# Kernel tuning notes

Measured on AMD Instinct MI355X. Metric: run time of the kernel, lower is better.

The kernel has to match this reference:

```python
import jax, jax.numpy as jnp
import numpy as np

B, S, D, H, F = 4, 1024, 1024, 16, 4096
DH = D // H
EPS = 1e-5


def _ln(x, g, b):
    mu = jnp.mean(x, axis=-1, keepdims=True)
    var = jnp.mean((x - mu) ** 2, axis=-1, keepdims=True)
    return (x - mu) * jax.lax.rsqrt(var + EPS) * g + b


def _mha(q_in, k_in, v_in, mask, wq, bq, wk, bk, wv, bv, wo, bo):
    b, sq, d = q_in.shape
    sk = k_in.shape[1]
    Q = (q_in @ wq + bq).reshape(b, sq, H, DH).transpose(0, 2, 1, 3)  # [B,H,Sq,dh]
    K = (k_in @ wk + bk).reshape(b, sk, H, DH).transpose(0, 2, 1, 3)
    V = (v_in @ wv + bv).reshape(b, sk, H, DH).transpose(0, 2, 1, 3)
    scores = jnp.einsum('bhqd,bhkd->bhqk', Q, K) / jnp.sqrt(jnp.asarray(DH, Q.dtype))
    if mask is not None:
        scores = jnp.where(mask[:, None] == 0, jnp.asarray(-1e9, scores.dtype), scores)
    w = jax.nn.softmax(scores, axis=-1)
    ctx = jnp.einsum('bhqk,bhkd->bhqd', w, V).transpose(0, 2, 1, 3).reshape(b, sq, d)
    return ctx @ wo + bo


def setup_inputs() -> dict:
    key = jax.random.key(0)
    ks = jax.random.split(key, 20)
    s = 0.02
    inp = {
        'x': jax.random.normal(ks[0], (B, S, D), jnp.float32),
        'src_x': jax.random.normal(ks[1], (B, S, D), jnp.float32),
        # causal self-attention mask (1 = keep), cross mask all ones
        'mask': jnp.broadcast_to(jnp.tril(jnp.ones((S, S), jnp.int32)), (B, S, S)),
        'src_mask': jnp.ones((B, S, S), jnp.int32),
        'ln1_g': jnp.ones((D,), jnp.float32), 'ln1_b': jnp.zeros((D,), jnp.float32),
        'ln2_g': jnp.ones((D,), jnp.float32), 'ln2_b': jnp.zeros((D,), jnp.float32),
        'ln3_g': jnp.ones((D,), jnp.float32), 'ln3_b': jnp.zeros((D,), jnp.float32),
    }
    names = ['sa_wq', 'sa_wk', 'sa_wv', 'sa_wo', 'ca_wq', 'ca_wk', 'ca_wv', 'ca_wo']
    for i, n in enumerate(names):
        inp[n] = jax.random.normal(ks[2 + i], (D, D), jnp.float32) * s
        inp[n.replace('w', 'b')] = jnp.zeros((D,), jnp.float32)
    inp['ff_w1'] = jax.random.normal(ks[10], (D, F), jnp.float32) * s
    inp['ff_b1'] = jnp.zeros((F,), jnp.float32)
    inp['ff_w2'] = jax.random.normal(ks[11], (F, D), jnp.float32) * s
    inp['ff_b2'] = jnp.zeros((D,), jnp.float32)
    return inp


def reference(x, mask, src_x, src_mask,
              ln1_g, ln1_b, ln2_g, ln2_b, ln3_g, ln3_b,
              sa_wq, sa_bq, sa_wk, sa_bk, sa_wv, sa_bv, sa_wo, sa_bo,
              ca_wq, ca_bq, ca_wk, ca_bk, ca_wv, ca_bv, ca_wo, ca_bo,
              ff_w1, ff_b1, ff_w2, ff_b2):
    # pre-layer-norm decoder layer (dropout = 0 / eval mode)
    h = _ln(x, ln1_g, ln1_b)
    x = x + _mha(h, h, h, mask, sa_wq, sa_bq, sa_wk, sa_bk, sa_wv, sa_bv, sa_wo, sa_bo)
    h = _ln(x, ln2_g, ln2_b)
    x = x + _mha(h, src_x, src_x, src_mask, ca_wq, ca_bq, ca_wk, ca_bk, ca_wv, ca_bv, ca_wo, ca_bo)
    h = _ln(x, ln3_g, ln3_b)
    x = x + (jax.nn.relu(h @ ff_w1 + ff_b1) @ ff_w2 + ff_b2)
    return x
```

## Files before the change

### kernel.cpp

```cpp
#include <hip/hip_runtime.h>
#include <hip/hip_bf16.h>

#define B_ 4
#define S_ 1024
#define D_ 1024
#define H_ 16
#define DH_ 64
#define F_ 4096

typedef unsigned short u16;
typedef unsigned int u32;
typedef __attribute__((ext_vector_type(8))) short bf16x8;
typedef __attribute__((ext_vector_type(4))) short bf16x4;
typedef __attribute__((ext_vector_type(4))) float f32x4;

__device__ __forceinline__ float bf2f(u16 u) {
    return __uint_as_float(((u32)u) << 16);
}
__device__ __forceinline__ u16 f2bf(float f) {
    __hip_bfloat16 h = __float2bfloat16(f);
    return *reinterpret_cast<u16*>(&h);
}

typedef __attribute__((address_space(1))) const u32 gu32;
typedef __attribute__((address_space(3))) u32 lu32;
__device__ __forceinline__ void gl_lds16(const void* g, void* l) {
    __builtin_amdgcn_global_load_lds((gu32*)g, (lu32*)l, 16, 0, 0);
}

__global__ __launch_bounds__(256) void cvt1_kernel(const float* __restrict__ s,
                                                   u16* __restrict__ d) {
    int i = (blockIdx.x * 256 + threadIdx.x) * 4;
    float4 v = *(const float4*)(s + i);
    u16 o0 = f2bf(v.x), o1 = f2bf(v.y), o2 = f2bf(v.z), o3 = f2bf(v.w);
    d[i] = o0; d[i+1] = o1; d[i+2] = o2; d[i+3] = o3;
}

__device__ __forceinline__ void trcvt_body(const float* __restrict__ src,
                                           u16* __restrict__ dst, int K, int N,
                                           int n0, int k0) {
    __shared__ u16 tile[64][65];
    int t = threadIdx.x;
    int c = t & 63, r4 = t >> 6;
#pragma unroll
    for (int i = 0; i < 16; i++) {
        int r = i * 4 + r4;
        tile[c][r] = f2bf(src[(size_t)(k0 + r) * N + n0 + c]);
    }
    __syncthreads();
#pragma unroll
    for (int i = 0; i < 16; i++) {
        int rr = i * 4 + r4;
        dst[(size_t)(n0 + rr) * K + k0 + c] = tile[rr][c];
    }
}

__global__ __launch_bounds__(256) void trcvt_kernel(const float* __restrict__ src,
                                                    u16* __restrict__ dst,
                                                    int K, int N) {
    trcvt_body(src, dst, K, N, blockIdx.x * 64, blockIdx.y * 64);
}

struct TP { const float* src[8]; u16* dst[8]; };
__global__ __launch_bounds__(256) void trcvt8_kernel(TP tp) {
    trcvt_body(tp.src[blockIdx.z], tp.dst[blockIdx.z], D_, D_,
               blockIdx.x * 64, blockIdx.y * 64);
}

__global__ __launch_bounds__(256) void mask_reduce_kernel(const int* __restrict__ mask,
                                                          unsigned char* __restrict__ bmask) {
    int t = threadIdx.x;
    int qb = blockIdx.x >> 4, kb = blockIdx.x & 15, b = blockIdx.y;
    bool all1 = true, any1 = false;
#pragma unroll
    for (int i = 0; i < 16; i++) {
        int e = t + i * 256;
        int r = e >> 6, c = e & 63;
        int v = mask[((size_t)(b * S_ + qb * 64 + r)) * S_ + kb * 64 + c];
        all1 = all1 && (v != 0);
        any1 = any1 || (v != 0);
    }
    unsigned long long ba = __ballot(all1), bn = __ballot(any1);
    __shared__ unsigned long long sa[4], sn[4];
    if ((t & 63) == 0) { sa[t >> 6] = ba; sn[t >> 6] = bn; }
    __syncthreads();
    if (t == 0) {
        bool A = ((sa[0] & sa[1] & sa[2] & sa[3]) == ~0ull);
        bool Y = ((sn[0] | sn[1] | sn[2] | sn[3]) != 0ull);
        bmask[b * 256 + blockIdx.x] = A ? 2 : (Y ? 1 : 0);
    }
}

template<bool COPY>
__global__ __launch_bounds__(256) void ln_kernel(const float* __restrict__ xin,
                                                 const float* __restrict__ g,
                                                 const float* __restrict__ bta,
                                                 float* xcur,
                                                 u16* __restrict__ hout) {
    int row = blockIdx.x;
    int t = threadIdx.x;
    size_t base = (size_t)row * D_;
    float v[4];
#pragma unroll
    for (int i = 0; i < 4; i++) v[i] = xin[base + t + i * 256];
    float s  = v[0] + v[1] + v[2] + v[3];
    float s2 = v[0]*v[0] + v[1]*v[1] + v[2]*v[2] + v[3]*v[3];
#pragma unroll
    for (int m = 1; m < 64; m <<= 1) {
        s  += __shfl_xor(s, m);
        s2 += __shfl_xor(s2, m);
    }
    __shared__ float red[8];
    int wave = t >> 6;
    if ((t & 63) == 0) { red[wave*2] = s; red[wave*2+1] = s2; }
    __syncthreads();
    float fs  = red[0] + red[2] + red[4] + red[6];
    float fs2 = red[1] + red[3] + red[5] + red[7];
    float mu  = fs * (1.0f / D_);
    float var = fs2 * (1.0f / D_) - mu * mu;
    float rs  = rsqrtf(var + 1e-5f);
#pragma unroll
    for (int i = 0; i < 4; i++) {
        int c = t + i * 256;
        float x = v[i];
        if (COPY) xcur[base + c] = x;
        hout[base + c] = f2bf((x - mu) * rs * g[c] + bta[c]);
    }
}

struct Bias3 { const float* b0; const float* b1; const float* b2; int n1; int n2; };

__device__ __forceinline__ float bias_at(const Bias3& bs, int c) {
    const float* p; int o;
    if (c < bs.n1)      { p = bs.b0; o = c; }
    else if (c < bs.n2) { p = bs.b1; o = c - bs.n1; }
    else                { p = bs.b2; o = c - bs.n2; }
    return p[o];
}

template<int BM, int BN, int OUT_MODE, bool BIAS_ROW>
__global__ __launch_bounds__(256) void gemm128_kernel(const u16* __restrict__ A,
                                                      const u16* __restrict__ Bt,
                                                      Bias3 bias,
                                                      const float* res,
                                                      void* out,
                                                      int M, int N, int K) {
    constexpr int MT = (BM == 64) ? 4 : (BN == 64 ? 2 : 4);
    constexpr int NT = (BN == 64) ? 4 : (BM == 64 ? 2 : 4);
    __shared__ u16 As[2][BM * 64];
    __shared__ u16 Bs[2][BN * 64];
    int t = threadIdx.x;
    int m0 = blockIdx.y * BM, n0 = blockIdx.x * BN;
    int w = t >> 6, lane = t & 63, quad = lane >> 4, l16 = lane & 15;
    int wm, wn;
    if (BM == 128 && BN == 128) { wm = (w >> 1) * 64; wn = (w & 1) * 64; }
    else if (BN == 64)          { wm = w * 32;        wn = 0; }
    else                        { wm = 0;             wn = w * 32; }

    f32x4 acc[MT][NT] = {};
    int sr = lane >> 3;
    int gc = ((lane & 7) ^ sr) * 8;
    int x7 = l16 & 7;
    const u16* gA = A + (size_t)m0 * K;
    const u16* gB = Bt + (size_t)n0 * K;

    auto stage = [&](int k0, int buf) {
#pragma unroll
        for (int j = w; j < BM / 8; j += 4)
            gl_lds16(gA + (size_t)(j * 8 + sr) * K + k0 + gc, &As[buf][j * 512]);
#pragma unroll
        for (int j = w; j < BN / 8; j += 4)
            gl_lds16(gB + (size_t)(j * 8 + sr) * K + k0 + gc, &Bs[buf][j * 512]);
    };

    stage(0, 0);
    int cur = 0;
    for (int k0 = 0; k0 < K; k0 += 64) {
        __syncthreads();
        if (k0 + 64 < K) stage(k0 + 64, cur ^ 1);

#pragma unroll
        for (int s = 0; s < 2; s++) {
            bf16x8 af[MT], bfr[NT];
            int cp = ((s * 4 + quad) ^ x7) * 8;
#pragma unroll
            for (int mt = 0; mt < MT; mt++)
                af[mt] = *(const bf16x8*)&As[cur][(wm + mt * 16 + l16) * 64 + cp];
#pragma unroll
            for (int nt = 0; nt < NT; nt++)
                bfr[nt] = *(const bf16x8*)&Bs[cur][(wn + nt * 16 + l16) * 64 + cp];
#pragma unroll
            for (int mt = 0; mt < MT; mt++)
#pragma unroll
                for (int nt = 0; nt < NT; nt++)
                    acc[mt][nt] = __builtin_amdgcn_mfma_f32_16x16x32_bf16(af[mt], bfr[nt], acc[mt][nt], 0, 0, 0);
        }
        cur ^= 1;
    }

#pragma unroll
    for (int nt = 0; nt < NT; nt++) {
        int col = n0 + wn + nt * 16 + l16;
        float bc = BIAS_ROW ? 0.f : bias_at(bias, col);
#pragma unroll
        for (int mt = 0; mt < MT; mt++) {
#pragma unroll
            for (int r = 0; r < 4; r++) {
                int row = m0 + wm + mt * 16 + quad * 4 + r;
                float v = acc[mt][nt][r] + (BIAS_ROW ? bias_at(bias, row) : bc);
                if (OUT_MODE == 1) v = fmaxf(v, 0.f);
                if (OUT_MODE == 2) {
                    v += res[(size_t)row * N + col];
                    ((float*)out)[(size_t)row * N + col] = v;
                } else {
                    ((u16*)out)[(size_t)row * N + col] = f2bf(v);
                }
            }
        }
    }
}

__global__ __launch_bounds__(256) void attn_kernel(const u16* __restrict__ Q, int ldq,
                                                   const u16* __restrict__ Kb, int ldk,
                                                   const u16* __restrict__ Vt,
                                                   const int* __restrict__ mask,
                                                   const unsigned char* __restrict__ bmask,
                                                   u16* __restrict__ ctx) {
    __shared__ u16 Ks[2][2][64 * 64];
    __shared__ u16 Vs[2][2][64 * 64];
    int t = threadIdx.x;
    int b = blockIdx.z, hh = blockIdx.y;
    int w = t >> 6, lane = t & 63, quad = lane >> 4, l16 = lane & 15;
    int hoff = hh * DH_;

    int qt[2] = { (int)blockIdx.x, 15 - (int)blockIdx.x };

    bf16x8 ones8;
#pragma unroll
    for (int j = 0; j < 8; j++) ones8[j] = (short)0x3F80;

    bf16x8 qf[2][2];
#pragma unroll
    for (int tt = 0; tt < 2; tt++) {
        int qrow = qt[tt] * 64 + w * 16 + l16;
#pragma unroll
        for (int kk = 0; kk < 2; kk++) {
            bf16x8 v = *(const bf16x8*)(Q + (size_t)(b * S_ + qrow) * ldq + hoff + kk * 32 + quad * 8);
#pragma unroll
            for (int j = 0; j < 8; j++)
                v[j] = (short)f2bf(bf2f((u16)v[j]) * 0.125f);
            qf[tt][kk] = v;
        }
    }

    f32x4 oacc[2][4] = {};
    f32x4 lacc[2] = {};

    unsigned nz[2], mx[2];
#pragma unroll
    for (int tt = 0; tt < 2; tt++) {
        nz[tt] = 0; mx[tt] = 0;
        for (int c = 0; c < 16; c++) {
            int v = bmask ? (int)bmask[(b * 16 + qt[tt]) * 16 + c] : 1;
            if (v)      nz[tt] |= 1u << c;
            if (v == 1) mx[tt] |= 1u << c;
        }
    }
    unsigned nzU = nz[0] | nz[1];
    unsigned remS = 0;
    for (int s = 0; s < 8; s++) if ((nzU >> (2 * s)) & 3u) remS |= 1u << s;

    int sr = lane >> 3;
    int gc = ((lane & 7) ^ sr) * 8;

    auto stage64 = [&](int c, int buf) {
        int k0 = c * 64, c64 = c & 1;
        for (int j = w; j < 8; j += 4) {
            gl_lds16(Kb + (size_t)(b * S_ + k0 + j * 8 + sr) * ldk + hoff + gc, &Ks[buf][c64][j * 512]);
            gl_lds16(Vt + (size_t)(hoff + j * 8 + sr) * (B_ * S_) + b * S_ + k0 + gc, &Vs[buf][c64][j * 512]);
        }
    };
    auto stageS = [&](int s, int buf) {
        if ((nzU >> (2 * s)) & 1u)     stage64(2 * s, buf);
        if ((nzU >> (2 * s + 1)) & 1u) stage64(2 * s + 1, buf);
    };

    int cur = 0;
    int s = remS ? __builtin_ctz(remS) : 8;
    if (s < 8) stageS(s, 0);

    while (s < 8) {
        remS &= remS - 1;
        int ns = remS ? __builtin_ctz(remS) : 8;
        __syncthreads();
        if (ns < 8) stageS(ns, cur ^ 1);

#pragma unroll
        for (int c64 = 0; c64 < 2; c64++) {
            int c = 2 * s + c64;
            if (!((nzU >> c) & 1u)) continue;
            int k0c = c * 64;
            const u16* KsT = &Ks[cur][c64][0];
            const u16* VsT = &Vs[cur][c64][0];

#pragma unroll
            for (int tt = 0; tt < 2; tt++) {
                if (!((nz[tt] >> c) & 1u)) continue;
                bool mixed = (mx[tt] >> c) & 1u;

                float p[4][4];
#pragma unroll
                for (int nt = 0; nt < 4; nt++) {
                    f32x4 sacc = {};
                    int krow = nt * 16 + l16;
#pragma unroll
                    for (int kk = 0; kk < 2; kk++) {
                        int cp = ((kk * 4 + quad) ^ (krow & 7)) * 8;
                        bf16x8 kf = *(const bf16x8*)&KsT[krow * 64 + cp];
                        sacc = __builtin_amdgcn_mfma_f32_16x16x32_bf16(kf, qf[tt][kk], sacc, 0, 0, 0);
                    }
#pragma unroll
                    for (int r = 0; r < 4; r++) {
                        float sv = sacc[r];
                        if (mixed) {
                            int qq = qt[tt] * 64 + w * 16 + l16;
                            int kc = k0c + nt * 16 + quad * 4 + r;
                            if (mask[(size_t)(b * S_ + qq) * S_ + kc] == 0) sv = -1e9f;
                        }
                        p[nt][r] = __expf(fminf(sv, 20.f));
                    }
                }

#pragma unroll
                for (int mp = 0; mp < 2; mp++) {
                    bf16x8 af;
#pragma unroll
                    for (int r = 0; r < 4; r++) {
                        af[r]     = (short)f2bf(p[2 * mp][r]);
                        af[4 + r] = (short)f2bf(p[2 * mp + 1][r]);
                    }
                    lacc[tt] = __builtin_amdgcn_mfma_f32_16x16x32_bf16(af, ones8, lacc[tt], 0, 0, 0);
#pragma unroll
                    for (int dt = 0; dt < 4; dt++) {
                        int vrow = dt * 16 + l16;
                        int ch0 = ((2 * mp) * 2 + (quad >> 1)) ^ (vrow & 7);
                        int ch1 = ((2 * mp + 1) * 2 + (quad >> 1)) ^ (vrow & 7);
                        int off = (quad & 1) * 4;
                        bf16x4 lo = *(const bf16x4*)&VsT[vrow * 64 + ch0 * 8 + off];
                        bf16x4 hi = *(const bf16x4*)&VsT[vrow * 64 + ch1 * 8 + off];
                        bf16x8 vf;
#pragma unroll
                        for (int j = 0; j < 4; j++) { vf[j] = lo[j]; vf[4 + j] = hi[j]; }
                        oacc[tt][dt] = __builtin_amdgcn_mfma_f32_16x16x32_bf16(af, vf, oacc[tt][dt], 0, 0, 0);
                    }
                }
            }
        }
        s = ns;
        cur ^= 1;
    }

#pragma unroll
    for (int tt = 0; tt < 2; tt++)
#pragma unroll
        for (int dt = 0; dt < 4; dt++)
#pragma unroll
            for (int r = 0; r < 4; r++) {
                int qq = qt[tt] * 64 + w * 16 + quad * 4 + r;
                float l = lacc[tt][r];
                float inv = l > 0.f ? 1.f / l : 0.f;
                ctx[(size_t)(b * S_ + qq) * D_ + hoff + dt * 16 + l16] = f2bf(oacc[tt][dt][r] * inv);
            }
}

extern "C" void kernel_launch(void* const* d_in, const int* in_sizes, int n_in,
                              void* d_out, int out_size, void* d_ws, size_t ws_size,
                              hipStream_t stream) {
    const float* x     = (const float*)d_in[0];
    const float* srcx  = (const float*)d_in[1];
    const int*   mask  = (const int*)d_in[2];
    const int*   smask = (const int*)d_in[3];
    const float* ln1g = (const float*)d_in[4],  *ln1b = (const float*)d_in[5];
    const float* ln2g = (const float*)d_in[6],  *ln2b = (const float*)d_in[7];
    const float* ln3g = (const float*)d_in[8],  *ln3b = (const float*)d_in[9];
    const float* sa_wq = (const float*)d_in[10], *sa_bq = (const float*)d_in[11];
    const float* sa_wk = (const float*)d_in[12], *sa_bk = (const float*)d_in[13];
    const float* sa_wv = (const float*)d_in[14], *sa_bv = (const float*)d_in[15];
    const float* sa_wo = (const float*)d_in[16], *sa_bo = (const float*)d_in[17];
    const float* ca_wq = (const float*)d_in[18], *ca_bq = (const float*)d_in[19];
    const float* ca_wk = (const float*)d_in[20], *ca_bk = (const float*)d_in[21];
    const float* ca_wv = (const float*)d_in[22], *ca_bv = (const float*)d_in[23];
    const float* ca_wo = (const float*)d_in[24], *ca_bo = (const float*)d_in[25];
    const float* ff_w1 = (const float*)d_in[26], *ff_b1 = (const float*)d_in[27];
    const float* ff_w2 = (const float*)d_in[28], *ff_b2 = (const float*)d_in[29];

    char* ws = (char*)d_ws;
    const size_t MB = 1ull << 20;
    const size_t DD = (size_t)D_ * D_;
    float* xcur = (float*)ws;
    u16* h     = (u16*)(ws + 16 * MB);
    u16* qk    = (u16*)(ws + 24 * MB);
    u16* qb    = (u16*)(ws + 24 * MB);
    u16* kbuf  = (u16*)(ws + 32 * MB);
    u16* vt    = (u16*)(ws + 40 * MB);
    u16* ctx   = (u16*)(ws + 48 * MB);
    u16* ff    = (u16*)(ws + 24 * MB);
    u16* sxb   = (u16*)(ws + 56 * MB);
    u16* wqk_s = (u16*)(ws + 64 * MB);
    u16* wv_s  = (u16*)(ws + 68 * MB);
    u16* wo_s  = (u16*)(ws + 70 * MB);
    u16* wq_c  = (u16*)(ws + 72 * MB);
    u16* wk_c  = (u16*)(ws + 74 * MB);
    u16* wv_c  = (u16*)(ws + 76 * MB);
    u16* wo_c  = (u16*)(ws + 78 * MB);
    u16* wff1  = (u16*)(ws + 80 * MB);
    u16* wff2  = (u16*)(ws + 88 * MB);
    unsigned char* bm_self = nullptr, *bm_cross = nullptr;
    if (ws_size >= 96 * MB + 8192) {
        bm_self  = (unsigned char*)(ws + ws_size - 8192);
        bm_cross = bm_self + 4096;
    }

    dim3 blk(256);

    TP tp = {{sa_wq, sa_wk, sa_wv, sa_wo, ca_wq, ca_wk, ca_wv, ca_wo},
             {wqk_s, wqk_s + DD, wv_s, wo_s, wq_c, wk_c, wv_c, wo_c}};
    trcvt8_kernel<<<dim3(16, 16, 8), blk, 0, stream>>>(tp);
    trcvt_kernel<<<dim3(F_ / 64, D_ / 64), blk, 0, stream>>>(ff_w1, wff1, D_, F_);
    trcvt_kernel<<<dim3(D_ / 64, F_ / 64), blk, 0, stream>>>(ff_w2, wff2, F_, D_);
    cvt1_kernel<<<B_ * S_ * D_ / 1024, blk, 0, stream>>>(srcx, sxb);
    if (bm_self) {
        mask_reduce_kernel<<<dim3(256, B_), blk, 0, stream>>>(mask, bm_self);
        mask_reduce_kernel<<<dim3(256, B_), blk, 0, stream>>>(smask, bm_cross);
    }

    Bias3 bqk = { sa_bq, sa_bk, sa_bk, 1024, 2048 };
    Bias3 bsv = { sa_bv, sa_bv, sa_bv, 1 << 30, 1 << 30 };
    Bias3 bso = { sa_bo, sa_bo, sa_bo, 1 << 30, 1 << 30 };
    Bias3 bcq = { ca_bq, ca_bq, ca_bq, 1 << 30, 1 << 30 };
    Bias3 bck = { ca_bk, ca_bk, ca_bk, 1 << 30, 1 << 30 };
    Bias3 bcv = { ca_bv, ca_bv, ca_bv, 1 << 30, 1 << 30 };
    Bias3 bco = { ca_bo, ca_bo, ca_bo, 1 << 30, 1 << 30 };
    Bias3 bf1 = { ff_b1, ff_b1, ff_b1, 1 << 30, 1 << 30 };
    Bias3 bf2 = { ff_b2, ff_b2, ff_b2, 1 << 30, 1 << 30 };

    ln_kernel<true><<<B_ * S_, blk, 0, stream>>>(x, ln1g, ln1b, xcur, h);
    gemm128_kernel<128,128,0,false><<<dim3(16, 32), blk, 0, stream>>>(h, wqk_s, bqk, nullptr, qk, 4096, 2048, 1024);
    gemm128_kernel<64,128,0,true><<<dim3(32, 16), blk, 0, stream>>>(wv_s, h, bsv, nullptr, vt, 1024, 4096, 1024);
    attn_kernel<<<dim3(8, H_, B_), blk, 0, stream>>>(qk, 2048, qk + 1024, 2048, vt, mask, bm_self, ctx);
    gemm128_kernel<128,64,2,false><<<dim3(16, 32), blk, 0, stream>>>(ctx, wo_s, bso, xcur, xcur, 4096, 1024, 1024);

    ln_kernel<false><<<B_ * S_, blk, 0, stream>>>(xcur, ln2g, ln2b, nullptr, h);
    gemm128_kernel<128,64,0,false><<<dim3(16, 32), blk, 0, stream>>>(h, wq_c, bcq, nullptr, qb, 4096, 1024, 1024);
    gemm128_kernel<128,64,0,false><<<dim3(16, 32), blk, 0, stream>>>(sxb, wk_c, bck, nullptr, kbuf, 4096, 1024, 1024);
    gemm128_kernel<64,128,0,true><<<dim3(32, 16), blk, 0, stream>>>(wv_c, sxb, bcv, nullptr, vt, 1024, 4096, 1024);
    attn_kernel<<<dim3(8, H_, B_), blk, 0, stream>>>(qb, 1024, kbuf, 1024, vt, smask, bm_cross, ctx);
    gemm128_kernel<128,64,2,false><<<dim3(16, 32), blk, 0, stream>>>(ctx, wo_c, bco, xcur, xcur, 4096, 1024, 1024);

    ln_kernel<false><<<B_ * S_, blk, 0, stream>>>(xcur, ln3g, ln3b, nullptr, h);
    gemm128_kernel<128,128,1,false><<<dim3(32, 32), blk, 0, stream>>>(h, wff1, bf1, nullptr, ff, 4096, 4096, 1024);
    gemm128_kernel<128,64,2,false><<<dim3(16, 32), blk, 0, stream>>>(ff, wff2, bf2, xcur, (float*)d_out, 4096, 1024, 4096);
}
```

Baseline: 575.8 us.

## Split-K the FFN2 GEMM, batch cross Q/K GEMMs, add MFMA priority hints

The FFN down-projection (K=4096) now runs as a two-way split-K GEMM with 128x128 tiles writing fp32 partials, followed by a reduce kernel that adds the bias and residual. The cross-attention Q and K projections are merged into one launch using blockIdx.z. s_setprio hints are placed around the MFMA sections in the attention kernel. The aim is to shorten the serial K loop, cut launch count and improve wave scheduling, at the cost of extra fp32 partial traffic and one more reduce pass.

```diff
diff --git a/kernel.cpp b/kernel.cpp
--- a/kernel.cpp
+++ b/kernel.cpp
@@ -139,12 +139,13 @@
 }
 
 template<int BM, int BN, int OUT_MODE, bool BIAS_ROW>
-__global__ __launch_bounds__(256) void gemm128_kernel(const u16* __restrict__ A,
-                                                      const u16* __restrict__ Bt,
-                                                      Bias3 bias,
-                                                      const float* res,
-                                                      void* out,
-                                                      int M, int N, int K) {
+__device__ __forceinline__ void gemm128_body(const u16* __restrict__ A,
+                                             const u16* __restrict__ Bt,
+                                             Bias3 bias,
+                                             const float* res,
+                                             void* out,
+                                             int M, int N, int K,
+                                             int lda, int ldb) {
     constexpr int MT = (BM == 64) ? 4 : (BN == 64 ? 2 : 4);
     constexpr int NT = (BN == 64) ? 4 : (BM == 64 ? 2 : 4);
     __shared__ u16 As[2][BM * 64];
@@ -161,16 +162,16 @@
     int sr = lane >> 3;
     int gc = ((lane & 7) ^ sr) * 8;
     int x7 = l16 & 7;
-    const u16* gA = A + (size_t)m0 * K;
-    const u16* gB = Bt + (size_t)n0 * K;
+    const u16* gA = A + (size_t)m0 * lda;
+    const u16* gB = Bt + (size_t)n0 * ldb;
 
     auto stage = [&](int k0, int buf) {
 #pragma unroll
         for (int j = w; j < BM / 8; j += 4)
-            gl_lds16(gA + (size_t)(j * 8 + sr) * K + k0 + gc, &As[buf][j * 512]);
+            gl_lds16(gA + (size_t)(j * 8 + sr) * lda + k0 + gc, &As[buf][j * 512]);
 #pragma unroll
         for (int j = w; j < BN / 8; j += 4)
-            gl_lds16(gB + (size_t)(j * 8 + sr) * K + k0 + gc, &Bs[buf][j * 512]);
+            gl_lds16(gB + (size_t)(j * 8 + sr) * ldb + k0 + gc, &Bs[buf][j * 512]);
     };
 
     stage(0, 0);
@@ -201,16 +202,19 @@
 #pragma unroll
     for (int nt = 0; nt < NT; nt++) {
         int col = n0 + wn + nt * 16 + l16;
-        float bc = BIAS_ROW ? 0.f : bias_at(bias, col);
+        float bc = (OUT_MODE == 3) ? 0.f : (BIAS_ROW ? 0.f : bias_at(bias, col));
 #pragma unroll
         for (int mt = 0; mt < MT; mt++) {
 #pragma unroll
             for (int r = 0; r < 4; r++) {
                 int row = m0 + wm + mt * 16 + quad * 4 + r;
-                float v = acc[mt][nt][r] + (BIAS_ROW ? bias_at(bias, row) : bc);
+                float v = acc[mt][nt][r] + bc;
+                if (OUT_MODE != 3 && BIAS_ROW) v += bias_at(bias, row);
                 if (OUT_MODE == 1) v = fmaxf(v, 0.f);
                 if (OUT_MODE == 2) {
                     v += res[(size_t)row * N + col];
+                    ((float*)out)[(size_t)row * N + col] = v;
+                } else if (OUT_MODE == 3) {
                     ((float*)out)[(size_t)row * N + col] = v;
                 } else {
                     ((u16*)out)[(size_t)row * N + col] = f2bf(v);
@@ -218,6 +222,62 @@
             }
         }
     }
+}
+
+template<int BM, int BN, int OUT_MODE, bool BIAS_ROW>
+__global__ __launch_bounds__(256) void gemm128_kernel(const u16* __restrict__ A,
+                                                      const u16* __restrict__ Bt,
+                                                      Bias3 bias,
+                                                      const float* res,
+                                                      void* out,
+                                                      int M, int N, int K) {
+    gemm128_body<BM, BN, OUT_MODE, BIAS_ROW>(A, Bt, bias, res, out, M, N, K, K, K);
+}
+
+__global__ __launch_bounds__(256) void gemm128_splitk2_kernel(const u16* __restrict__ A,
+                                                              const u16* __restrict__ Bt,
+                                                              float* __restrict__ p0,
+                                                              float* __restrict__ p1,
+                                                              int M, int N, int Kh, int ld) {
+    int z = blockIdx.z;
+    Bias3 dummy = { nullptr, nullptr, nullptr, 1 << 30, 1 << 30 };
+    gemm128_body<128, 128, 3, false>(A + z * Kh, Bt + z * Kh, dummy, nullptr,
+                                     z ? (void*)p1 : (void*)p0, M, N, Kh, ld, ld);
+}
+
+__global__ __launch_bounds__(256) void ffn2_reduce_kernel(const float* __restrict__ p0,
+                                                          const float* __restrict__ p1,
+                                                          const float* __restrict__ b2,
+                                                          const float* __restrict__ res,
+                                                          float* __restrict__ out) {
+    int i = (blockIdx.x * 256 + threadIdx.x) * 4;
+    int col = i & (D_ - 1);
+    float4 a = *(const float4*)(p0 + i);
+    float4 b = *(const float4*)(p1 + i);
+    float4 r = *(const float4*)(res + i);
+    float4 bb = *(const float4*)(b2 + col);
+    float4 o;
+    o.x = a.x + b.x + r.x + bb.x;
+    o.y = a.y + b.y + r.y + bb.y;
+    o.z = a.z + b.z + r.z + bb.z;
+    o.w = a.w + b.w + r.w + bb.w;
+    *(float4*)(out + i) = o;
+}
+
+struct Pair2 {
+    const u16* A0; const u16* A1;
+    const u16* B0; const u16* B1;
+    const float* b0; const float* b1;
+    u16* o0; u16* o1;
+};
+__global__ __launch_bounds__(256) void gemm128_pairqk_kernel(Pair2 p, int M, int N, int K) {
+    int z = blockIdx.z;
+    const u16* A  = z ? p.A1 : p.A0;
+    const u16* Bt = z ? p.B1 : p.B0;
+    const float* bb = z ? p.b1 : p.b0;
+    u16* o = z ? p.o1 : p.o0;
+    Bias3 bs = { bb, bb, bb, 1 << 30, 1 << 30 };
+    gemm128_body<128, 64, 0, false>(A, Bt, bs, nullptr, o, M, N, K, K, K);
 }
 
 __global__ __launch_bounds__(256) void attn_kernel(const u16* __restrict__ Q, int ldq,
@@ -313,12 +373,14 @@
                 for (int nt = 0; nt < 4; nt++) {
                     f32x4 sacc = {};
                     int krow = nt * 16 + l16;
+                    __builtin_amdgcn_s_setprio(1);
 #pragma unroll
                     for (int kk = 0; kk < 2; kk++) {
                         int cp = ((kk * 4 + quad) ^ (krow & 7)) * 8;
                         bf16x8 kf = *(const bf16x8*)&KsT[krow * 64 + cp];
                         sacc = __builtin_amdgcn_mfma_f32_16x16x32_bf16(kf, qf[tt][kk], sacc, 0, 0, 0);
                     }
+                    __builtin_amdgcn_s_setprio(0);
 #pragma unroll
                     for (int r = 0; r < 4; r++) {
                         float sv = sacc[r];
@@ -339,6 +401,7 @@
                         af[r]     = (short)f2bf(p[2 * mp][r]);
                         af[4 + r] = (short)f2bf(p[2 * mp + 1][r]);
                     }
+                    __builtin_amdgcn_s_setprio(1);
                     lacc[tt] = __builtin_amdgcn_mfma_f32_16x16x32_bf16(af, ones8, lacc[tt], 0, 0, 0);
 #pragma unroll
                     for (int dt = 0; dt < 4; dt++) {
@@ -353,6 +416,7 @@
                         for (int j = 0; j < 4; j++) { vf[j] = lo[j]; vf[4 + j] = hi[j]; }
                         oacc[tt][dt] = __builtin_amdgcn_mfma_f32_16x16x32_bf16(af, vf, oacc[tt][dt], 0, 0, 0);
                     }
+                    __builtin_amdgcn_s_setprio(0);
                 }
             }
         }
@@ -415,6 +479,8 @@
     u16* wo_c  = (u16*)(ws + 78 * MB);
     u16* wff1  = (u16*)(ws + 80 * MB);
     u16* wff2  = (u16*)(ws + 88 * MB);
+    float* fp0 = (float*)(ws + 56 * MB);
+    float* fp1 = (float*)(ws + 72 * MB);
     unsigned char* bm_self = nullptr, *bm_cross = nullptr;
     if (ws_size >= 96 * MB + 8192) {
         bm_self  = (unsigned char*)(ws + ws_size - 8192);
@@ -437,12 +503,9 @@
     Bias3 bqk = { sa_bq, sa_bk, sa_bk, 1024, 2048 };
     Bias3 bsv = { sa_bv, sa_bv, sa_bv, 1 << 30, 1 << 30 };
     Bias3 bso = { sa_bo, sa_bo, sa_bo, 1 << 30, 1 << 30 };
-    Bias3 bcq = { ca_bq, ca_bq, ca_bq, 1 << 30, 1 << 30 };
-    Bias3 bck = { ca_bk, ca_bk, ca_bk, 1 << 30, 1 << 30 };
     Bias3 bcv = { ca_bv, ca_bv, ca_bv, 1 << 30, 1 << 30 };
     Bias3 bco = { ca_bo, ca_bo, ca_bo, 1 << 30, 1 << 30 };
     Bias3 bf1 = { ff_b1, ff_b1, ff_b1, 1 << 30, 1 << 30 };
-    Bias3 bf2 = { ff_b2, ff_b2, ff_b2, 1 << 30, 1 << 30 };
 
     ln_kernel<true><<<B_ * S_, blk, 0, stream>>>(x, ln1g, ln1b, xcur, h);
     gemm128_kernel<128,128,0,false><<<dim3(16, 32), blk, 0, stream>>>(h, wqk_s, bqk, nullptr, qk, 4096, 2048, 1024);
@@ -451,13 +514,16 @@
     gemm128_kernel<128,64,2,false><<<dim3(16, 32), blk, 0, stream>>>(ctx, wo_s, bso, xcur, xcur, 4096, 1024, 1024);
 
     ln_kernel<false><<<B_ * S_, blk, 0, stream>>>(xcur, ln2g, ln2b, nullptr, h);
-    gemm128_kernel<128,64,0,false><<<dim3(16, 32), blk, 0, stream>>>(h, wq_c, bcq, nullptr, qb, 4096, 1024, 1024);
-    gemm128_kernel<128,64,0,false><<<dim3(16, 32), blk, 0, stream>>>(sxb, wk_c, bck, nullptr, kbuf, 4096, 1024, 1024);
+    {
+        Pair2 pqk = { h, sxb, wq_c, wk_c, ca_bq, ca_bk, qb, kbuf };
+        gemm128_pairqk_kernel<<<dim3(16, 32, 2), blk, 0, stream>>>(pqk, 4096, 1024, 1024);
+    }
     gemm128_kernel<64,128,0,true><<<dim3(32, 16), blk, 0, stream>>>(wv_c, sxb, bcv, nullptr, vt, 1024, 4096, 1024);
     attn_kernel<<<dim3(8, H_, B_), blk, 0, stream>>>(qb, 1024, kbuf, 1024, vt, smask, bm_cross, ctx);
     gemm128_kernel<128,64,2,false><<<dim3(16, 32), blk, 0, stream>>>(ctx, wo_c, bco, xcur, xcur, 4096, 1024, 1024);
 
     ln_kernel<false><<<B_ * S_, blk, 0, stream>>>(xcur, ln3g, ln3b, nullptr, h);
     gemm128_kernel<128,128,1,false><<<dim3(32, 32), blk, 0, stream>>>(h, wff1, bf1, nullptr, ff, 4096, 4096, 1024);
-    gemm128_kernel<128,64,2,false><<<dim3(16, 32), blk, 0, stream>>>(ff, wff2, bf2, xcur, (float*)d_out, 4096, 1024, 4096);
-}
+    gemm128_splitk2_kernel<<<dim3(8, 32, 2), blk, 0, stream>>>(ff, wff2, fp0, fp1, 4096, 1024, 2048, 4096);
+    ffn2_reduce_kernel<<<dim3(B_ * S_ * D_ / 1024), blk, 0, stream>>>(fp0, fp1, ff_b2, xcur, (float*)d_out);
+}
```

After: 566.8 us. Within noise of the previous version (-1.6%).
